# Optimization experiments

Measured on AMD Instinct MI355X. Metric: run time of the kernel, lower is better.

Reference implementation:

```python
import jax, jax.numpy as jnp
import numpy as np

B, T, C, H, HD = 2, 2048, 768, 12, 64


def setup_inputs() -> dict:
    key = jax.random.key(0)
    k0, k1, k2, k3 = jax.random.split(key, 4)
    x = jax.random.normal(k0, (B, T, C), dtype=jnp.float32)
    w_attn = jax.random.normal(k1, (3 * H * HD, C), dtype=jnp.float32) * 0.02
    b_attn = jnp.zeros((3 * H * HD,), dtype=jnp.float32)
    w_proj = jax.random.normal(k2, (C, H * HD), dtype=jnp.float32) * 0.02
    b_proj = jnp.zeros((C,), dtype=jnp.float32)
    sel_w = jax.random.normal(k3, (H,), dtype=jnp.float32) * 0.3
    return {"x": x, "w_attn": w_attn, "b_attn": b_attn,
            "w_proj": w_proj, "b_proj": b_proj, "sel_w": sel_w}


def reference(x, w_attn, b_attn, w_proj, b_proj, sel_w):
    Bc, Tc, Cc = x.shape
    Hc = sel_w.shape[0]
    HDc = w_attn.shape[0] // (3 * Hc)
    qkv = x @ w_attn.T + b_attn                          # [B,T,3*H*HD]
    q, k, v = jnp.split(qkv, 3, axis=2)
    q = q.reshape(Bc, Tc, Hc, HDc).transpose(0, 2, 1, 3)  # [B,H,T,HD]
    k = k.reshape(Bc, Tc, Hc, HDc).transpose(0, 2, 1, 3)
    v = v.reshape(Bc, Tc, Hc, HDc).transpose(0, 2, 1, 3)

    scale = 1.0 / np.sqrt(HDc).astype(np.float32)
    att = jnp.einsum('bhid,bhjd->bhij', q, k) * scale    # [B,H,T,T]
    causal = jnp.tril(jnp.ones((Tc, Tc), dtype=bool))
    neg_inf = jnp.asarray(-jnp.inf, dtype=att.dtype)
    att = jnp.where(causal[None, None], att, neg_inf)

    # selection head: per-head linear combo of (causally-zeroed) logits
    att0 = jnp.where(causal[None, None], att, 0.0)       # -inf -> 0 before combo
    S = jnp.einsum('bhij,h->bij', att0, sel_w)           # [B,T,T], bias=False
    S = jnp.where(causal[None], S, 0.0)
    S = jax.nn.relu(S)
    S = S.at[..., 0].set(0.0)                            # protect_bos_token
    S = S * (1.0 - jnp.eye(Tc, dtype=S.dtype))           # prevent_from_masking_myself

    FF = jnp.cumsum(S, axis=-2)                          # forgetting accumulation over rows
    FF_shifted = jnp.concatenate(
        [jnp.zeros_like(FF[..., :1, :]), FF[..., :-1, :]], axis=-2)

    att = jax.nn.softmax(att - FF_shifted[:, None], axis=-1)
    y = jnp.einsum('bhij,bhjd->bhid', att, v)            # [B,H,T,HD]
    y = y.transpose(0, 2, 1, 3).reshape(Bc, Tc, Hc * HDc)
    return y @ w_proj.T + b_proj
```

## Files before the change

### kernel.cpp

```cpp
#include <hip/hip_runtime.h>

#define B_   2
#define T_   2048
#define C_   768
#define H_   12
#define HD_  64
#define M_   (B_ * T_)
#define N3_  (3 * C_)
#define KB_  (C_ * 2)

typedef __bf16 bf16_t;
typedef bf16_t bf16x8 __attribute__((ext_vector_type(8)));
typedef float  floatx4 __attribute__((ext_vector_type(4)));

__device__ inline floatx4 mfma_bf16(bf16x8 a, bf16x8 b, floatx4 c) {
    return __builtin_amdgcn_mfma_f32_16x16x32_bf16(a, b, c, 0, 0, 0);
}

__device__ __forceinline__ void async_copy16(const void* g, void* l) {
    __builtin_amdgcn_global_load_lds(
        (const __attribute__((address_space(1))) void*)g,
        (__attribute__((address_space(3))) void*)l, 16, 0, 0);
}

__device__ __forceinline__ void stage8k(const char* tile, char* ldsbase,
                                        int k0b, int wave, int lane) {
#pragma unroll
    for (int i = 0; i < 2; ++i) {
        int p = (wave * 2 + i) * 64 + lane;
        int r = p >> 2, slot = p & 3;
        int g = slot ^ ((r >> 1) & 3);
        async_copy16(tile + (size_t)r * KB_ + k0b + g * 16, ldsbase + p * 16);
    }
}

__device__ __forceinline__ bf16x8 frag_read(const char* ldsbase, int row, int quad) {
    int slot = quad ^ ((row >> 1) & 3);
    return *(const bf16x8*)(ldsbase + row * 64 + slot * 16);
}

template<bool TRIPLE>
__device__ __forceinline__ void gemm_loop(
    const char* Ah, const char* Al, const char* Bh, const char* Bl,
    char* lds, floatx4 (&acc)[4][4])
{
    int tid = threadIdx.x, lane = tid & 63, wave = tid >> 6;
    int l15 = lane & 15, quad = lane >> 4;
    int wr = wave >> 1, wc = wave & 1;
    const int PH = TRIPLE ? 32768 : 16384;
    auto stage = [&](int ph, int k0) {
        char* base = lds + ph * PH;
        stage8k(Ah, base, k0, wave, lane);
        stage8k(Bh, base + 8192, k0, wave, lane);
        if (TRIPLE) {
            stage8k(Al, base + 16384, k0, wave, lane);
            stage8k(Bl, base + 24576, k0, wave, lane);
        }
    };
    stage(0, 0);
    int ph = 0;
#pragma unroll 1
    for (int k0 = 0; k0 < KB_; k0 += 64) {
        __syncthreads();
        if (k0 + 64 < KB_) stage(ph ^ 1, k0 + 64);
        char* base = lds + ph * PH;
        bf16x8 ah[4], al[4], bh[4], bl[4];
#pragma unroll
        for (int t = 0; t < 4; ++t) {
            ah[t] = frag_read(base,         wr * 64 + t * 16 + l15, quad);
            bh[t] = frag_read(base + 8192,  wc * 64 + t * 16 + l15, quad);
            if (TRIPLE) {
                al[t] = frag_read(base + 16384, wr * 64 + t * 16 + l15, quad);
                bl[t] = frag_read(base + 24576, wc * 64 + t * 16 + l15, quad);
            }
        }
#pragma unroll
        for (int mi = 0; mi < 4; ++mi)
#pragma unroll
            for (int ni = 0; ni < 4; ++ni) {
                acc[mi][ni] = mfma_bf16(ah[mi], bh[ni], acc[mi][ni]);
                if (TRIPLE) {
                    acc[mi][ni] = mfma_bf16(ah[mi], bl[ni], acc[mi][ni]);
                    acc[mi][ni] = mfma_bf16(al[mi], bh[ni], acc[mi][ni]);
                }
            }
        ph ^= 1;
    }
}

__global__ __launch_bounds__(256) void split_f32(
    const float* __restrict__ src, bf16_t* __restrict__ hi,
    bf16_t* __restrict__ lo, int n)
{
    int i = blockIdx.x * 256 + threadIdx.x;
    if (i < n) {
        float f = src[i];
        bf16_t h = (bf16_t)f;
        hi[i] = h;
        lo[i] = (bf16_t)(f - (float)h);
    }
}

__global__ __launch_bounds__(256) void conv_f32(
    const float* __restrict__ src, bf16_t* __restrict__ dst, int n)
{
    int i = blockIdx.x * 256 + threadIdx.x;
    if (i < n) dst[i] = (bf16_t)src[i];
}

__global__ __launch_bounds__(256) void qkv_gemm(
    const bf16_t* __restrict__ x_hi, const bf16_t* __restrict__ x_lo,
    const bf16_t* __restrict__ w_hi, const bf16_t* __restrict__ w_lo,
    const float* __restrict__ bias, const float* __restrict__ selw,
    bf16_t* __restrict__ q_hi, bf16_t* __restrict__ q_lo,
    bf16_t* __restrict__ kw_hi, bf16_t* __restrict__ kw_lo,
    bf16_t* __restrict__ k_b, bf16_t* __restrict__ v_b)
{
    extern __shared__ char lds[];
    int m0 = blockIdx.x * 128, n0 = blockIdx.y * 128;
    floatx4 acc[4][4];
#pragma unroll
    for (int i = 0; i < 4; ++i)
#pragma unroll
        for (int j = 0; j < 4; ++j) acc[i][j] = (floatx4){0.f, 0.f, 0.f, 0.f};
    if (n0 >= 2 * C_) {
        gemm_loop<false>((const char*)(x_hi + (size_t)m0 * C_), nullptr,
                         (const char*)(w_hi + (size_t)n0 * C_), nullptr, lds, acc);
    } else {
        gemm_loop<true>((const char*)(x_hi + (size_t)m0 * C_),
                        (const char*)(x_lo + (size_t)m0 * C_),
                        (const char*)(w_hi + (size_t)n0 * C_),
                        (const char*)(w_lo + (size_t)n0 * C_), lds, acc);
    }

    int tid = threadIdx.x, lane = tid & 63, wave = tid >> 6;
    int l15 = lane & 15, quad = lane >> 4;
    int wr = wave >> 1, wc = wave & 1;
    int cb = n0 + wc * 64;
#pragma unroll
    for (int ni = 0; ni < 4; ++ni) {
        int col = cb + ni * 16 + l15;
        float bb = bias[col];
#pragma unroll
        for (int mi = 0; mi < 4; ++mi)
#pragma unroll
            for (int r = 0; r < 4; ++r) {
                int row = m0 + wr * 64 + mi * 16 + quad * 4 + r;
                float v = acc[mi][ni][r] + bb;
                if (cb < C_) {
                    float vs = v * 0.125f;
                    bf16_t h = (bf16_t)vs;
                    q_hi[(size_t)row * C_ + col] = h;
                    q_lo[(size_t)row * C_ + col] = (bf16_t)(vs - (float)h);
                } else if (cb < 2 * C_) {
                    int c2 = col - C_;
                    k_b[(size_t)row * C_ + c2] = (bf16_t)v;
                    float kw = v * selw[c2 >> 6];
                    bf16_t h = (bf16_t)kw;
                    kw_hi[(size_t)row * C_ + c2] = h;
                    kw_lo[(size_t)row * C_ + c2] = (bf16_t)(kw - (float)h);
                } else {
                    v_b[(size_t)row * C_ + (col - 2 * C_)] = (bf16_t)v;
                }
            }
    }
}

#define SEG_    16
#define SEGLEN_ (T_ / SEG_)

__global__ __launch_bounds__(256) void s_gemm(
    const bf16_t* __restrict__ q_hi, const bf16_t* __restrict__ q_lo,
    const bf16_t* __restrict__ kw_hi, const bf16_t* __restrict__ kw_lo,
    float* __restrict__ SF, float* __restrict__ segsum)
{
    extern __shared__ char lds[];
    int t = blockIdx.x, b = blockIdx.z;
    int it = (int)((sqrtf(8.f * t + 1.f) - 1.f) * 0.5f);
    while ((it + 1) * (it + 2) / 2 <= t) ++it;
    while (it * (it + 1) / 2 > t) --it;
    int jt = t - it * (it + 1) / 2;
    int i0 = it * 128, j0 = jt * 128;
    float* out = SF + (size_t)b * T_ * T_;

    floatx4 acc[4][4];
#pragma unroll
    for (int i = 0; i < 4; ++i)
#pragma unroll
        for (int j = 0; j < 4; ++j) acc[i][j] = (floatx4){0.f, 0.f, 0.f, 0.f};
    size_t arow = ((size_t)b * T_ + i0) * C_;
    size_t brow = ((size_t)b * T_ + j0) * C_;
    gemm_loop<true>((const char*)(q_hi + arow), (const char*)(q_lo + arow),
                    (const char*)(kw_hi + brow), (const char*)(kw_lo + brow),
                    lds, acc);

    int tid = threadIdx.x, lane = tid & 63, wave = tid >> 6;
    int l15 = lane & 15, quad = lane >> 4;
    int wr = wave >> 1, wc = wave & 1;
    float colsum[4] = {0.f, 0.f, 0.f, 0.f};
#pragma unroll
    for (int ni = 0; ni < 4; ++ni) {
        int j = j0 + wc * 64 + ni * 16 + l15;
#pragma unroll
        for (int mi = 0; mi < 4; ++mi)
#pragma unroll
            for (int r = 0; r < 4; ++r) {
                int i = i0 + wr * 64 + mi * 16 + quad * 4 + r;
                float s = acc[mi][ni][r];
                s = (j >= 1 && j < i) ? fmaxf(s, 0.f) : 0.f;
                out[(size_t)i * T_ + j] = s;
                colsum[ni] += s;
            }
    }
#pragma unroll
    for (int ni = 0; ni < 4; ++ni) {
        colsum[ni] += __shfl_xor(colsum[ni], 16);
        colsum[ni] += __shfl_xor(colsum[ni], 32);
    }
    float* red = (float*)lds;
    if (quad == 0) {
#pragma unroll
        for (int ni = 0; ni < 4; ++ni)
            red[wr * 128 + wc * 64 + ni * 16 + l15] = colsum[ni];
    }
    __syncthreads();
    if (wave < 2) {
        float ssum = red[wave * 64 + lane] + red[128 + wave * 64 + lane];
        segsum[((size_t)b * SEG_ + it) * T_ + j0 + wave * 64 + lane] = ssum;
    }
}

__global__ __launch_bounds__(256) void scan_seg_excl(float* __restrict__ segsum)
{
    int gid = blockIdx.x * 256 + threadIdx.x;
    int j = gid & (T_ - 1);
    int b = gid >> 11;
    float run = 0.f;
#pragma unroll
    for (int s = 0; s < SEG_; ++s) {
        size_t idx = ((size_t)b * SEG_ + s) * T_ + j;
        float v = (s * SEGLEN_ + SEGLEN_ - 1 <= j) ? 0.f : segsum[idx];
        segsum[idx] = run;
        run += v;
    }
}

__global__ __launch_bounds__(256) void scan_apply(
    float* __restrict__ SF, const float* __restrict__ segsum)
{
    int gid  = blockIdx.x * 256 + threadIdx.x;
    int j    = gid & (T_ - 1);
    int rest = gid >> 11;
    int seg  = rest & (SEG_ - 1);
    int b    = rest >> 4;
    if (seg * SEGLEN_ + SEGLEN_ - 1 < j) return;
    float run = segsum[((size_t)b * SEG_ + seg) * T_ + j];
    float* col = SF + (size_t)b * T_ * T_ + (size_t)(seg * SEGLEN_) * T_ + j;
#pragma unroll 4
    for (int i = 0; i < SEGLEN_; ++i) {
        float s = col[(size_t)i * T_];
        s = (seg * SEGLEN_ + i > j) ? s : 0.f;
        col[(size_t)i * T_] = run;
        run += s;
    }
}

__global__ __launch_bounds__(256) void vt_kernel(
    const bf16_t* __restrict__ v_b, bf16_t* __restrict__ vt)
{
    __shared__ bf16_t tile[64][72];
    int t0 = blockIdx.x * 64, h = blockIdx.y, b = blockIdx.z;
    int tid = threadIdx.x;
    int r = tid >> 2, sl = tid & 3;
    const bf16_t* src = v_b + ((size_t)(b * T_ + t0 + r)) * C_ + h * HD_ + sl * 16;
    *(int4*)&tile[r][sl * 16]     = *(const int4*)src;
    *(int4*)&tile[r][sl * 16 + 8] = *(const int4*)(src + 8);
    __syncthreads();
    int hd = tid >> 2, q = tid & 3;
#pragma unroll
    for (int half = 0; half < 2; ++half) {
        int c0 = (q * 2 + half) * 8;
        union { int4 i4; bf16_t e[8]; } u;
#pragma unroll
        for (int kk = 0; kk < 8; ++kk) u.e[kk] = tile[c0 + kk][hd];
        *(int4*)(vt + ((size_t)(b * H_ + h) * HD_ + hd) * T_ + t0 + c0) = u.i4;
    }
}

__global__ __launch_bounds__(256) void attn_kernel(
    const bf16_t* __restrict__ q_b, const bf16_t* __restrict__ k_b,
    const bf16_t* __restrict__ vt_g, const float* __restrict__ FF,
    bf16_t* __restrict__ y_b)
{
    __shared__ __align__(16) char KL[2][8192];
    __shared__ __align__(16) char VL[2][8192];
    __shared__ __align__(16) float LS[4][16][68];

    int tid = threadIdx.x, lane = tid & 63, wave = tid >> 6;
    int l15 = lane & 15, quad = lane >> 4;
    int bi = (int)gridDim.x - 1 - (int)blockIdx.x;
    int h = blockIdx.y, b = blockIdx.z;
    int i0w = bi * 64 + wave * 16;
    int jmax = bi * 64 + 63;
    const floatx4 fzero = {0.f, 0.f, 0.f, 0.f};

    const bf16_t* qrow = q_b + ((size_t)b * T_ + i0w + l15) * C_ + h * HD_;
    bf16x8 qa0 = *(const bf16x8*)(qrow + quad * 8);
    bf16x8 qa1 = *(const bf16x8*)(qrow + 32 + quad * 8);

    const bf16_t* kbase = k_b + (size_t)b * T_ * C_ + h * HD_;
    const bf16_t* vbase = vt_g + (size_t)(b * H_ + h) * HD_ * T_;
    const float*  fp    = FF + ((size_t)b * T_ + i0w + l15) * T_ + quad * 8;

    auto stage = [&](int ph, int j0) {
#pragma unroll
        for (int i = 0; i < 2; ++i) {
            int p = (wave * 2 + i) * 64 + lane;
            int r = p >> 3, sp = p & 7, s = sp ^ (r & 7);
            async_copy16(kbase + (size_t)(j0 + r) * C_ + s * 8, &KL[ph][p * 16]);
        }
#pragma unroll
        for (int i = 0; i < 2; ++i) {
            int p = (wave * 2 + i) * 64 + lane;
            int r = p >> 3, sp = p & 7, s = sp ^ (r & 7);
            async_copy16(vbase + (size_t)r * T_ + j0 + s * 8, &VL[ph][p * 16]);
        }
    };

    float m_run = -__builtin_inff(), l_run = 0.f;
    floatx4 O[4];
#pragma unroll
    for (int nt = 0; nt < 4; ++nt) O[nt] = fzero;

    stage(0, 0);
    int ph = 0;
#pragma unroll 1
    for (int j0 = 0; j0 <= jmax; j0 += 64) {
        __syncthreads();
        if (j0 + 64 <= jmax) stage(ph ^ 1, j0 + 64);

        float ffv[16];
        *(floatx4*)&ffv[0]  = *(const floatx4*)(fp);
        *(floatx4*)&ffv[4]  = *(const floatx4*)(fp + 4);
        *(floatx4*)&ffv[8]  = *(const floatx4*)(fp + 32);
        *(floatx4*)&ffv[12] = *(const floatx4*)(fp + 36);
        fp += 64;

        floatx4 pc[4];
#pragma unroll
        for (int s = 0; s < 4; ++s) {
            int r = s * 16 + l15;
            bf16x8 k0 = *(const bf16x8*)&KL[ph][r * 128 + ((quad     ^ (r & 7)) * 16)];
            bf16x8 k1 = *(const bf16x8*)&KL[ph][r * 128 + (((quad+4) ^ (r & 7)) * 16)];
            floatx4 p = mfma_bf16(qa0, k0, fzero);
            pc[s] = mfma_bf16(qa1, k1, p);
        }
#pragma unroll
        for (int s = 0; s < 4; ++s)
#pragma unroll
            for (int r = 0; r < 4; ++r)
                LS[wave][quad * 4 + r][s * 16 + l15] = pc[s][r];
        float qk[16];
        *(floatx4*)&qk[0]  = *(const floatx4*)&LS[wave][l15][quad * 8];
        *(floatx4*)&qk[4]  = *(const floatx4*)&LS[wave][l15][quad * 8 + 4];
        *(floatx4*)&qk[8]  = *(const floatx4*)&LS[wave][l15][32 + quad * 8];
        *(floatx4*)&qk[12] = *(const floatx4*)&LS[wave][l15][32 + quad * 8 + 4];

        float lg[16];
#pragma unroll
        for (int c = 0; c < 16; ++c) lg[c] = qk[c] - ffv[c];
        if (j0 + 63 > i0w) {
            int i = i0w + l15;
#pragma unroll
            for (int c = 0; c < 16; ++c) {
                int j = j0 + (c >> 3) * 32 + quad * 8 + (c & 7);
                lg[c] = (j <= i) ? lg[c] : -__builtin_inff();
            }
        }
        float rm = lg[0];
#pragma unroll
        for (int c = 1; c < 16; ++c) rm = fmaxf(rm, lg[c]);
        rm = fmaxf(rm, __shfl_xor(rm, 16));
        rm = fmaxf(rm, __shfl_xor(rm, 32));
        float mn = fmaxf(m_run, rm);
        float mnu = fmaxf(mn, -1e30f);
        float alpha = __expf(m_run - mnu);
        float p[16], ps = 0.f;
#pragma unroll
        for (int c = 0; c < 16; ++c) { p[c] = __expf(lg[c] - mnu); ps += p[c]; }
        ps += __shfl_xor(ps, 16);
        ps += __shfl_xor(ps, 32);
        l_run = l_run * alpha + ps;
        m_run = mn;
#pragma unroll
        for (int r = 0; r < 4; ++r) {
            float ar = __shfl(alpha, quad * 4 + r);
#pragma unroll
            for (int nt = 0; nt < 4; ++nt) O[nt][r] *= ar;
        }
        bf16x8 pa0, pa1;
#pragma unroll
        for (int c = 0; c < 8; ++c) { pa0[c] = (bf16_t)p[c]; pa1[c] = (bf16_t)p[8 + c]; }
#pragma unroll
        for (int nt = 0; nt < 4; ++nt) {
            int r = nt * 16 + l15;
            bf16x8 v0 = *(const bf16x8*)&VL[ph][r * 128 + ((quad     ^ (r & 7)) * 16)];
            bf16x8 v1 = *(const bf16x8*)&VL[ph][r * 128 + (((quad+4) ^ (r & 7)) * 16)];
            O[nt] = mfma_bf16(pa0, v0, O[nt]);
            O[nt] = mfma_bf16(pa1, v1, O[nt]);
        }
        ph ^= 1;
    }

#pragma unroll
    for (int r = 0; r < 4; ++r) {
        float inv = 1.f / __shfl(l_run, quad * 4 + r);
        int i = i0w + quad * 4 + r;
#pragma unroll
        for (int nt = 0; nt < 4; ++nt)
            y_b[((size_t)b * T_ + i) * C_ + h * HD_ + nt * 16 + l15] =
                (bf16_t)(O[nt][r] * inv);
    }
}

__global__ __launch_bounds__(256) void proj_gemm(
    const bf16_t* __restrict__ y_b, const bf16_t* __restrict__ wp_b,
    const float* __restrict__ bias, float* __restrict__ out)
{
    extern __shared__ char lds[];
    int m0 = blockIdx.x * 128, n0 = blockIdx.y * 128;
    floatx4 acc[4][4];
#pragma unroll
    for (int i = 0; i < 4; ++i)
#pragma unroll
        for (int j = 0; j < 4; ++j) acc[i][j] = (floatx4){0.f, 0.f, 0.f, 0.f};
    gemm_loop<false>((const char*)(y_b + (size_t)m0 * C_), nullptr,
                     (const char*)(wp_b + (size_t)n0 * C_), nullptr, lds, acc);

    int tid = threadIdx.x, lane = tid & 63, wave = tid >> 6;
    int l15 = lane & 15, quad = lane >> 4;
    int wr = wave >> 1, wc = wave & 1;
#pragma unroll
    for (int ni = 0; ni < 4; ++ni) {
        int col = n0 + wc * 64 + ni * 16 + l15;
        float bb = bias[col];
#pragma unroll
        for (int mi = 0; mi < 4; ++mi)
#pragma unroll
            for (int r = 0; r < 4; ++r)
                out[(size_t)(m0 + wr * 64 + mi * 16 + quad * 4 + r) * C_ + col] =
                    acc[mi][ni][r] + bb;
    }
}

extern "C" void kernel_launch(void* const* d_in, const int* in_sizes, int n_in,
                              void* d_out, int out_size, void* d_ws, size_t ws_size,
                              hipStream_t stream)
{
    const float* x      = (const float*)d_in[0];
    const float* w_attn = (const float*)d_in[1];
    const float* b_attn = (const float*)d_in[2];
    const float* w_proj = (const float*)d_in[3];
    const float* b_proj = (const float*)d_in[4];
    const float* sel_w  = (const float*)d_in[5];
    float* out = (float*)d_out;

    char* ws = (char*)d_ws;
    size_t off = 0;
    auto alloc = [&](size_t bytes) {
        void* p = ws + off;
        off += (bytes + 255) & ~(size_t)255;
        return p;
    };
    const size_t MC2 = (size_t)M_ * C_ * 2;
    bf16_t* q_hi   = (bf16_t*)alloc(MC2);
    bf16_t* q_lo   = (bf16_t*)alloc(MC2);
    bf16_t* kw_hi  = (bf16_t*)alloc(MC2);
    bf16_t* kw_lo  = (bf16_t*)alloc(MC2);
    bf16_t* k_b    = (bf16_t*)alloc(MC2);
    bf16_t* v_b    = (bf16_t*)alloc(MC2);
    bf16_t* y_b    = (bf16_t*)alloc(MC2);
    bf16_t* wp_b   = (bf16_t*)alloc((size_t)C_ * C_ * 2);
    float*  segsum = (float*)alloc((size_t)B_ * SEG_ * T_ * 4);
    char* shared_base = (char*)alloc((size_t)B_ * T_ * T_ * 4);
    bf16_t* x_hi = (bf16_t*)shared_base;
    bf16_t* x_lo = (bf16_t*)(shared_base + MC2);
    bf16_t* w_hi = (bf16_t*)(shared_base + 2 * MC2);
    bf16_t* w_lo = (bf16_t*)(shared_base + 2 * MC2 + (size_t)N3_ * C_ * 2);
    float*  SF   = (float*)shared_base;
    bf16_t* vt   = kw_hi;

    int nx = M_ * C_, nw = N3_ * C_, np = C_ * C_;
    split_f32<<<dim3((nx + 255) / 256), 256, 0, stream>>>(x, x_hi, x_lo, nx);
    split_f32<<<dim3((nw + 255) / 256), 256, 0, stream>>>(w_attn, w_hi, w_lo, nw);
    conv_f32<<<dim3((np + 255) / 256), 256, 0, stream>>>(w_proj, wp_b, np);

    qkv_gemm<<<dim3(M_ / 128, N3_ / 128), 256, 65536, stream>>>(
        x_hi, x_lo, w_hi, w_lo, b_attn, sel_w,
        q_hi, q_lo, kw_hi, kw_lo, k_b, v_b);
    s_gemm<<<dim3(136, 1, B_), 256, 65536, stream>>>(
        q_hi, q_lo, kw_hi, kw_lo, SF, segsum);
    vt_kernel<<<dim3(T_ / 64, H_, B_), 256, 0, stream>>>(v_b, vt);
    scan_seg_excl<<<dim3(B_ * T_ / 256), 256, 0, stream>>>(segsum);
    scan_apply<<<dim3(B_ * SEG_ * T_ / 256), 256, 0, stream>>>(SF, segsum);
    attn_kernel<<<dim3(T_ / 64, H_, B_), 256, 0, stream>>>(q_hi, k_b, vt, SF, y_b);
    proj_gemm<<<dim3(M_ / 128, C_ / 128), 256, 32768, stream>>>(y_b, wp_b, b_proj, out);
}
```

Before: 282.1 us.

## Run softmax in MFMA accumulator layout and transpose only bf16 probabilities via LDS

The attention kernel now does the masking, online-softmax max/sum and rescaling directly in the MFMA output layout, keeping per-row running state for 4 rows per lane. Previously the fp32 logits were transposed through LDS first. Now only the bf16 probabilities are written to a swizzled LDS buffer and read back as the A operand for the PV MFMA, halving LDS traffic and dropping the alpha shuffles. In exchange, the FF bias loads become scalar strided loads instead of float4 vectors, and row reductions need 4-step shuffles per row instead of 2.

```diff
diff --git a/kernel.cpp b/kernel.cpp
--- a/kernel.cpp
+++ b/kernel.cpp
@@ -294,7 +294,7 @@
 {
     __shared__ __align__(16) char KL[2][8192];
     __shared__ __align__(16) char VL[2][8192];
-    __shared__ __align__(16) float LS[4][16][68];
+    __shared__ __align__(16) bf16_t LSP[4][1024];
 
     int tid = threadIdx.x, lane = tid & 63, wave = tid >> 6;
     int l15 = lane & 15, quad = lane >> 4;
@@ -310,7 +310,10 @@
 
     const bf16_t* kbase = k_b + (size_t)b * T_ * C_ + h * HD_;
     const bf16_t* vbase = vt_g + (size_t)(b * H_ + h) * HD_ * T_;
-    const float*  fp    = FF + ((size_t)b * T_ + i0w + l15) * T_ + quad * 8;
+    const float* fpr[4];
+#pragma unroll
+    for (int r = 0; r < 4; ++r)
+        fpr[r] = FF + ((size_t)b * T_ + i0w + quad * 4 + r) * T_ + l15;
 
     auto stage = [&](int ph, int j0) {
 #pragma unroll
@@ -327,8 +330,10 @@
         }
     };
 
-    float m_run = -__builtin_inff(), l_run = 0.f;
+    float m_run[4], l_run[4];
     floatx4 O[4];
+#pragma unroll
+    for (int r = 0; r < 4; ++r) { m_run[r] = -__builtin_inff(); l_run[r] = 0.f; }
 #pragma unroll
     for (int nt = 0; nt < 4; ++nt) O[nt] = fzero;
 
@@ -339,12 +344,13 @@
         __syncthreads();
         if (j0 + 64 <= jmax) stage(ph ^ 1, j0 + 64);
 
-        float ffv[16];
-        *(floatx4*)&ffv[0]  = *(const floatx4*)(fp);
-        *(floatx4*)&ffv[4]  = *(const floatx4*)(fp + 4);
-        *(floatx4*)&ffv[8]  = *(const floatx4*)(fp + 32);
-        *(floatx4*)&ffv[12] = *(const floatx4*)(fp + 36);
-        fp += 64;
+        float ff[4][4];
+#pragma unroll
+        for (int r = 0; r < 4; ++r) {
+#pragma unroll
+            for (int s = 0; s < 4; ++s) ff[s][r] = fpr[r][s * 16];
+            fpr[r] += 64;
+        }
 
         floatx4 pc[4];
 #pragma unroll
@@ -355,52 +361,57 @@
             floatx4 p = mfma_bf16(qa0, k0, fzero);
             pc[s] = mfma_bf16(qa1, k1, p);
         }
+
+        float lg[4][4];
+        bool diag = (j0 + 63 > i0w);
+#pragma unroll
+        for (int s = 0; s < 4; ++s) {
+            int j = j0 + s * 16 + l15;
+#pragma unroll
+            for (int r = 0; r < 4; ++r) {
+                float v = pc[s][r] - ff[s][r];
+                if (diag) v = (j <= i0w + quad * 4 + r) ? v : -__builtin_inff();
+                lg[s][r] = v;
+            }
+        }
+
+        float p[4][4];
+#pragma unroll
+        for (int r = 0; r < 4; ++r) {
+            float rm = fmaxf(fmaxf(lg[0][r], lg[1][r]), fmaxf(lg[2][r], lg[3][r]));
+#pragma unroll
+            for (int d = 1; d < 16; d <<= 1) rm = fmaxf(rm, __shfl_xor(rm, d));
+            float mn = fmaxf(m_run[r], rm);
+            float mnu = fmaxf(mn, -1e30f);
+            float alpha = __expf(m_run[r] - mnu);
+            float ps = 0.f;
+#pragma unroll
+            for (int s = 0; s < 4; ++s) {
+                p[s][r] = __expf(lg[s][r] - mnu);
+                ps += p[s][r];
+            }
+#pragma unroll
+            for (int d = 1; d < 16; d <<= 1) ps += __shfl_xor(ps, d);
+            l_run[r] = l_run[r] * alpha + ps;
+            m_run[r] = mn;
+#pragma unroll
+            for (int nt = 0; nt < 4; ++nt) O[nt][r] *= alpha;
+        }
+
+        bf16_t* LSb = &LSP[wave][0];
 #pragma unroll
         for (int s = 0; s < 4; ++s)
 #pragma unroll
-            for (int r = 0; r < 4; ++r)
-                LS[wave][quad * 4 + r][s * 16 + l15] = pc[s][r];
-        float qk[16];
-        *(floatx4*)&qk[0]  = *(const floatx4*)&LS[wave][l15][quad * 8];
-        *(floatx4*)&qk[4]  = *(const floatx4*)&LS[wave][l15][quad * 8 + 4];
-        *(floatx4*)&qk[8]  = *(const floatx4*)&LS[wave][l15][32 + quad * 8];
-        *(floatx4*)&qk[12] = *(const floatx4*)&LS[wave][l15][32 + quad * 8 + 4];
-
-        float lg[16];
-#pragma unroll
-        for (int c = 0; c < 16; ++c) lg[c] = qk[c] - ffv[c];
-        if (j0 + 63 > i0w) {
-            int i = i0w + l15;
-#pragma unroll
-            for (int c = 0; c < 16; ++c) {
-                int j = j0 + (c >> 3) * 32 + quad * 8 + (c & 7);
-                lg[c] = (j <= i) ? lg[c] : -__builtin_inff();
-            }
-        }
-        float rm = lg[0];
-#pragma unroll
-        for (int c = 1; c < 16; ++c) rm = fmaxf(rm, lg[c]);
-        rm = fmaxf(rm, __shfl_xor(rm, 16));
-        rm = fmaxf(rm, __shfl_xor(rm, 32));
-        float mn = fmaxf(m_run, rm);
-        float mnu = fmaxf(mn, -1e30f);
-        float alpha = __expf(m_run - mnu);
-        float p[16], ps = 0.f;
-#pragma unroll
-        for (int c = 0; c < 16; ++c) { p[c] = __expf(lg[c] - mnu); ps += p[c]; }
-        ps += __shfl_xor(ps, 16);
-        ps += __shfl_xor(ps, 32);
-        l_run = l_run * alpha + ps;
-        m_run = mn;
-#pragma unroll
-        for (int r = 0; r < 4; ++r) {
-            float ar = __shfl(alpha, quad * 4 + r);
-#pragma unroll
-            for (int nt = 0; nt < 4; ++nt) O[nt][r] *= ar;
-        }
-        bf16x8 pa0, pa1;
-#pragma unroll
-        for (int c = 0; c < 8; ++c) { pa0[c] = (bf16_t)p[c]; pa1[c] = (bf16_t)p[8 + c]; }
+            for (int r = 0; r < 4; ++r) {
+                int rr = quad * 4 + r;
+                int ch = (s * 2 + (l15 >> 3)) ^ (rr & 7);
+                LSb[rr * 64 + ch * 8 + (l15 & 7)] = (bf16_t)p[s][r];
+            }
+        asm volatile("s_waitcnt lgkmcnt(0)" ::: "memory");
+        int xk = l15 & 7;
+        bf16x8 pa0 = *(const bf16x8*)&LSb[l15 * 64 + ((quad ^ xk) * 8)];
+        bf16x8 pa1 = *(const bf16x8*)&LSb[l15 * 64 + (((4 + quad) ^ xk) * 8)];
+
 #pragma unroll
         for (int nt = 0; nt < 4; ++nt) {
             int r = nt * 16 + l15;
@@ -414,7 +425,7 @@
 
 #pragma unroll
     for (int r = 0; r < 4; ++r) {
-        float inv = 1.f / __shfl(l_run, quad * 4 + r);
+        float inv = 1.f / l_run[r];
         int i = i0w + quad * 4 + r;
 #pragma unroll
         for (int nt = 0; nt < 4; ++nt)
```

After: 301.0 us. +6.7%, slower.
